# Performance work log

Measured on AMD Instinct MI355X. Metric: run time of the kernel, lower is better.

Reference implementation:

```python
import jax, jax.numpy as jnp
import numpy as np
from jax import lax

EPS = 1e-5

def _ln(x, w, b):
    m = jnp.mean(x, axis=-1, keepdims=True)
    v = jnp.mean((x - m) ** 2, axis=-1, keepdims=True)
    return (x - m) / jnp.sqrt(v + EPS) * w + b

def setup_inputs() -> dict:
    key = jax.random.key(0)
    ks = jax.random.split(key, 16)
    B, H, W, C = 4, 128, 128, 96
    N = H * W
    hidden = 192          # int(2.0 * dim)
    qk = 48               # dim // 2
    x = jax.random.normal(ks[0], (B, N, C), dtype=jnp.float32)
    # LayerNorm params
    norm_w = jnp.ones((C,), jnp.float32); norm_b = jnp.zeros((C,), jnp.float32)
    n1_w = jnp.ones((C,), jnp.float32); n1_b = jnp.zeros((C,), jnp.float32)
    n2_w = jnp.ones((C,), jnp.float32); n2_b = jnp.zeros((C,), jnp.float32)
    # Linear weights stored as [in, out]
    Wh = jax.random.normal(ks[1], (C, hidden), jnp.float32) * 0.02
    bh = jnp.zeros((hidden,), jnp.float32)
    Wqk = jax.random.normal(ks[2], (C, qk), jnp.float32) * 0.02
    bqk = jnp.zeros((qk,), jnp.float32)
    proj_w = jax.random.normal(ks[3], (C, C), jnp.float32) * 0.02
    proj_b = jnp.zeros((C,), jnp.float32)
    # per-branch affine on qk (init: normal std 0.02 / zeros, as in torch code)
    g1 = jax.random.normal(ks[4], (2, qk), jnp.float32) * 0.02
    be1 = jnp.zeros((2, qk), jnp.float32)
    g2 = jax.random.normal(ks[5], (2, qk), jnp.float32) * 0.02
    be2 = jnp.zeros((2, qk), jnp.float32)
    # SR convs (OIHW), kaiming-like init fan_out = k*k*C
    sr1_w = jax.random.normal(ks[6], (C, C, 8, 8), jnp.float32) * np.sqrt(2.0 / (8 * 8 * C))
    sr1_b = jnp.zeros((C,), jnp.float32)
    sr2_w = jax.random.normal(ks[7], (C, C, 4, 4), jnp.float32) * np.sqrt(2.0 / (4 * 4 * C))
    sr2_b = jnp.zeros((C,), jnp.float32)
    return dict(x=x, H=H, W=W, norm_w=norm_w, norm_b=norm_b, Wh=Wh, bh=bh,
                Wqk=Wqk, bqk=bqk, g1=g1, be1=be1, g2=g2, be2=be2,
                sr1_w=sr1_w, sr1_b=sr1_b, sr2_w=sr2_w, sr2_b=sr2_b,
                n1_w=n1_w, n1_b=n1_b, n2_w=n2_w, n2_b=n2_b,
                proj_w=proj_w, proj_b=proj_b)

def _sr_branch(xmap, cw, cb, lw, lb, stride):
    # xmap: [B,C,H,W]; strided conv with kernel==stride, then LN+GELU over tokens
    y = lax.conv_general_dilated(xmap, cw, (stride, stride), 'VALID',
                                 dimension_numbers=('NCHW', 'OIHW', 'NCHW'))
    y = y + cb[:, None, None]
    B, C = y.shape[0], y.shape[1]
    y = y.reshape(B, C, -1).transpose(0, 2, 1)  # [B, N', C]
    return jax.nn.gelu(_ln(y, lw, lb), approximate=False)

def reference(x, H, W, norm_w, norm_b, Wh, bh, Wqk, bqk, g1, be1, g2, be2,
              sr1_w, sr1_b, sr2_w, sr2_b, n1_w, n1_b, n2_w, n2_b, proj_w, proj_b):
    B, N, C = x.shape
    half = C // 2  # C // num_heads with num_heads=2
    nx = _ln(x, norm_w, norm_b)
    h = jax.nn.silu(nx @ Wh + bh)              # [B,N,2C]
    v, gate = h[..., :C], h[..., C:]
    xmap = nx.transpose(0, 2, 1).reshape(B, C, H, W)
    x1 = _sr_branch(xmap, sr1_w, sr1_b, n1_w, n1_b, 8)   # [B, N/64, C]
    x2 = _sr_branch(xmap, sr2_w, sr2_b, n2_w, n2_b, 4)   # [B, N/16, C]
    Z1 = jax.nn.silu(x1 @ Wqk + bqk)           # [B,N1,qk]
    QK1 = Z1[..., None, :] * g1 + be1          # [B,N1,2,qk]
    q1, k1 = QK1[..., 0, :], QK1[..., 1, :]
    Z2 = jax.nn.silu(x2 @ Wqk + bqk)
    QK2 = Z2[..., None, :] * g2 + be2
    q2, k2 = QK2[..., 0, :], QK2[..., 1, :]
    inv_n = 1.0 / N
    a1 = jnp.einsum('bnd,bmd->bnm', v[..., :half], q1) * inv_n
    A1 = jnp.square(jax.nn.relu(a1))
    V1 = jnp.einsum('bnm,bmd->bnd', A1, k1)
    a2 = jnp.einsum('bnd,bmd->bnm', v[..., half:], q2) * inv_n
    A2 = jnp.square(jax.nn.relu(a2))
    V2 = jnp.einsum('bnm,bmd->bnd', A2, k2)
    xc = jnp.concatenate([V1, V2], axis=-1)    # [B,N,C]
    value = xc * gate
    out = value @ proj_w + proj_b
    return out + xc
```

## Files before the change

kernel.cpp:

```cpp
#include <hip/hip_runtime.h>
#include <math.h>

#define NB   4
#define IH   128
#define IW   128
#define NTOK 16384
#define CC   96
#define HID  192
#define QKD  48
#define EPSF 1e-5f
#define INV_N (1.0f/16384.0f)

typedef __attribute__((ext_vector_type(8))) short sh8;
typedef __attribute__((ext_vector_type(4))) short ush4;
typedef __attribute__((ext_vector_type(4))) float f32x4;

__device__ __forceinline__ float wave_sum64(float v){
    #pragma unroll
    for (int off = 32; off > 0; off >>= 1) v += __shfl_xor(v, off, 64);
    return v;
}
__device__ __forceinline__ float siluf(float x){ return x / (1.0f + __expf(-x)); }
__device__ __forceinline__ float geluf(float x){ return 0.5f*x*(1.0f + erff(x*0.7071067811865475f)); }

__device__ __forceinline__ unsigned short f2bf(float f){
    union { float f; unsigned u; } x; x.f = f;
    unsigned u = x.u + 0x7FFFu + ((x.u >> 16) & 1u);
    return (unsigned short)(u >> 16);
}
__device__ __forceinline__ float b2f(unsigned hi16){
    union { unsigned u; float f; } c; c.u = hi16; return c.f;
}
__device__ __forceinline__ unsigned cvtpk(float a, float b){
    unsigned r;
    asm("v_cvt_pk_bf16_f32 %0, %1, %2" : "=v"(r) : "v"(a), "v"(b));
    return r;
}
__device__ __forceinline__ void swap32(unsigned &x, unsigned &y){
    asm volatile("v_permlane32_swap_b32 %0, %1" : "+v"(x), "+v"(y));
}
__device__ __forceinline__ void swap16(unsigned &x, unsigned &y){
    asm volatile("v_permlane16_swap_b32 %0, %1" : "+v"(x), "+v"(y));
}

__global__ __launch_bounds__(256) void k_ln(const float* __restrict__ x,
                                            const float* __restrict__ w,
                                            const float* __restrict__ bb,
                                            unsigned short* __restrict__ nxbf,
                                            unsigned short* __restrict__ nxim,
                                            const float* __restrict__ s1, unsigned short* __restrict__ d1, int n1,
                                            const float* __restrict__ s2, unsigned short* __restrict__ d2, int n2){
    int bid = blockIdx.x;
    if (bid >= 16384){
        int i4 = ((bid - 16384)*256 + threadIdx.x)*4;
        if (i4 < n1){
            float4 v = *(const float4*)(s1 + i4);
            unsigned u0 = cvtpk(v.x, v.y), u1 = cvtpk(v.z, v.w);
            ush4 o = {(short)u0, (short)(u0>>16), (short)u1, (short)(u1>>16)};
            *(ush4*)(d1 + i4) = o;
        } else {
            int j = i4 - n1;
            if (j < n2){
                float4 v = *(const float4*)(s2 + j);
                unsigned u0 = cvtpk(v.x, v.y), u1 = cvtpk(v.z, v.w);
                ush4 o = {(short)u0, (short)(u0>>16), (short)u1, (short)(u1>>16)};
                *(ush4*)(d2 + j) = o;
            }
        }
        return;
    }
    __shared__ unsigned short tile[4][96];
    int r = threadIdx.x >> 6;
    int row = bid*4 + r;
    int l = threadIdx.x & 63;
    const float* xr = x + (size_t)row*CC;
    float a = xr[l];
    float b = (l < 32) ? xr[64+l] : 0.0f;
    float s = wave_sum64(a + b);
    float m = s * (1.0f/96.0f);
    float d1f = a - m;
    float d2f = b - m;
    float sq = d1f*d1f + ((l < 32) ? d2f*d2f : 0.0f);
    float var = wave_sum64(sq) * (1.0f/96.0f);
    float rstd = rsqrtf(var + EPSF);
    unsigned short b1 = f2bf(d1f*rstd*w[l] + bb[l]);
    nxbf[(size_t)row*CC + l] = b1;
    tile[r][l] = b1;
    if (l < 32){
        unsigned short b2 = f2bf(d2f*rstd*w[64+l] + bb[64+l]);
        nxbf[(size_t)row*CC + 64 + l] = b2;
        tile[r][64+l] = b2;
    }
    __syncthreads();
    int t = threadIdx.x;
    if (t < 96){
        int row0 = bid*4;
        int bb2 = row0 >> 14, hw = row0 & 16383;
        ush4 v = {(short)tile[0][t], (short)tile[1][t], (short)tile[2][t], (short)tile[3][t]};
        *(ush4*)(nxim + (((size_t)(bb2*96 + t)) << 14) + hw) = v;
    }
}

__device__ __forceinline__ void conv_body(const unsigned short* __restrict__ nxim,
                                          const unsigned short* __restrict__ wbf,
                                          float* __restrict__ part,
                                          int posLog, int pdimLog, int pszLog,
                                          int kTotal, int rb, int split,
                                          unsigned short* pt, unsigned short* wt){
    const int NCH = 6;
    int tid = threadIdx.x;
    int lane = tid & 63, wid = tid >> 6, lo = lane & 15, g = lane >> 4;
    int psz = 1 << pszLog, pdim = 1 << pdimLog;
    int ksLog = 2*pszLog;
    int kb0 = split * 384;
    int cinc = (64 >> ksLog) << 14;

    int j   = tid & 15;
    int coff = (j*4) >> ksLog;
    int s   = (j*4) & (psz*psz - 1);
    int sy  = s >> pszLog, sx = s & (psz-1);
    int pAddr[4], pOff[4];
    #pragma unroll
    for (int i = 0; i < 4; i++){
        int p = (tid >> 4) + 16*i;
        int R = rb*64 + p;
        int b = R >> posLog, pp = R & ((1 << posLog) - 1);
        int pi = pp >> pdimLog, pj = pp & (pdim-1);
        pAddr[i] = (((b*96 + coff) + (kb0 >> ksLog)) << 14) + (pi*psz + sy)*IW + pj*psz + sx;
        pOff[i]  = p*72 + j*4;
    }
    int jj = tid & 7;
    int wAddr[3], wOff[3];
    #pragma unroll
    for (int i = 0; i < 3; i++){
        int o = (tid >> 3) + 32*i;
        wAddr[i] = o*kTotal + kb0 + jj*8;
        wOff[i]  = o*72 + jj*8;
    }

    f32x4 acc[6];
    #pragma unroll
    for (int ct = 0; ct < 6; ct++) acc[ct] = (f32x4){0.f,0.f,0.f,0.f};

    ush4 pr[4]; sh8 wr[3];
    #pragma unroll
    for (int i = 0; i < 4; i++) pr[i] = *(const ush4*)(nxim + pAddr[i]);
    #pragma unroll
    for (int i = 0; i < 3; i++) wr[i] = *(const sh8*)(wbf + wAddr[i]);

    for (int ch = 0; ch < NCH; ch++){
        __syncthreads();
        #pragma unroll
        for (int i = 0; i < 4; i++) *(ush4*)&pt[pOff[i]] = pr[i];
        #pragma unroll
        for (int i = 0; i < 3; i++) *(sh8*)&wt[wOff[i]] = wr[i];
        if (ch < NCH-1){
            #pragma unroll
            for (int i = 0; i < 4; i++){ pAddr[i] += cinc; pr[i] = *(const ush4*)(nxim + pAddr[i]); }
            #pragma unroll
            for (int i = 0; i < 3; i++){ wAddr[i] += 64;  wr[i] = *(const sh8*)(wbf + wAddr[i]); }
        }
        __syncthreads();

        sh8 a0 = *(const sh8*)&pt[(wid*16 + lo)*72 + g*8];
        sh8 a1 = *(const sh8*)&pt[(wid*16 + lo)*72 + 32 + g*8];
        #pragma unroll
        for (int ct = 0; ct < 6; ct++){
            sh8 b0 = *(const sh8*)&wt[(ct*16 + lo)*72 + g*8];
            sh8 b1 = *(const sh8*)&wt[(ct*16 + lo)*72 + 32 + g*8];
            acc[ct] = __builtin_amdgcn_mfma_f32_16x16x32_bf16(a0, b0, acc[ct], 0, 0, 0);
            acc[ct] = __builtin_amdgcn_mfma_f32_16x16x32_bf16(a1, b1, acc[ct], 0, 0, 0);
        }
    }

    int rowsTotal = NB << posLog;
    #pragma unroll
    for (int ct = 0; ct < 6; ct++){
        int o = ct*16 + lo;
        #pragma unroll
        for (int jx = 0; jx < 4; jx++){
            int R = rb*64 + wid*16 + g*4 + jx;
            part[((size_t)split*rowsTotal + R)*96 + o] = acc[ct][jx];
        }
    }
}

__global__ __launch_bounds__(256) void k_mid(const unsigned short* __restrict__ nxbf,
                                             const unsigned short* __restrict__ nxim,
                                             const float* __restrict__ Wh,
                                             const float* __restrict__ bh,
                                             const unsigned short* __restrict__ w1bf,
                                             const unsigned short* __restrict__ w2bf,
                                             unsigned short* __restrict__ vbuf,
                                             unsigned short* __restrict__ gate,
                                             float* __restrict__ part1,
                                             float* __restrict__ part2){
    __shared__ unsigned short smem[192*100];
    int bid = blockIdx.x;
    if (bid < 512){
        unsigned short* pt = smem;
        unsigned short* wt = smem + 64*72;
        if (bid < 256) conv_body(nxim, w1bf, part1, 8, 4, 3, 6144, bid & 15, bid >> 4, pt, wt);
        else { int b2 = bid - 256; conv_body(nxim, w2bf, part2, 10, 5, 2, 1536, b2 & 63, b2 >> 6, pt, wt); }
        return;
    }
    unsigned short* whbf = smem;
    int tid  = threadIdx.x;
    int lane = tid & 63;
    int wid  = tid >> 6;
    int lo   = lane & 15;
    int g    = lane >> 4;
    int row0 = (bid - 512)*64 + wid*16;

    #pragma unroll
    for (int it = 0; it < 36; it++){
        int pidx = tid + it*256;
        int k = pidx / 96, cp = (pidx - k*96)*2;
        float2 v = *(const float2*)&Wh[k*HID + cp];
        unsigned u = cvtpk(v.x, v.y);
        whbf[cp*100 + k]     = (unsigned short)u;
        whbf[(cp+1)*100 + k] = (unsigned short)(u >> 16);
    }

    sh8 a[3];
    {
        const unsigned short* ar = nxbf + (size_t)(row0 + lo)*CC;
        #pragma unroll
        for (int kc = 0; kc < 3; kc++)
            a[kc] = *(const sh8*)(ar + kc*32 + g*8);
    }
    __syncthreads();

    f32x4 acc[12];
    #pragma unroll
    for (int ct = 0; ct < 12; ct++) acc[ct] = (f32x4){0.f,0.f,0.f,0.f};
    #pragma unroll
    for (int ct = 0; ct < 12; ct++){
        #pragma unroll
        for (int kc = 0; kc < 3; kc++){
            sh8 bw = *(const sh8*)&whbf[(ct*16 + lo)*100 + kc*32 + g*8];
            acc[ct] = __builtin_amdgcn_mfma_f32_16x16x32_bf16(a[kc], bw, acc[ct], 0, 0, 0);
        }
    }

    #pragma unroll
    for (int ct = 0; ct < 12; ct++){
        int col = ct*16 + lo;
        float bcol = bh[col];
        #pragma unroll
        for (int j = 0; j < 4; j++){
            size_t row = row0 + g*4 + j;
            float hv = siluf(acc[ct][j] + bcol);
            unsigned short hb = (unsigned short)cvtpk(hv, hv);
            if (col < 96) vbuf[row*CC + col] = hb;
            else          gate[row*CC + col - 96] = hb;
        }
    }
}

__global__ __launch_bounds__(64) void k_reduce(const float* __restrict__ part1,
                                               const float* __restrict__ part2,
                                               const float* __restrict__ cb1, const float* __restrict__ cb2,
                                               const float* __restrict__ lw1, const float* __restrict__ lw2,
                                               const float* __restrict__ lb1, const float* __restrict__ lb2,
                                               const float* __restrict__ wqk,
                                               const float* __restrict__ bqk,
                                               const float* __restrict__ g1, const float* __restrict__ g2,
                                               const float* __restrict__ be1, const float* __restrict__ be2,
                                               unsigned short* __restrict__ qp1, unsigned short* __restrict__ qp2,
                                               unsigned short* __restrict__ kt1, unsigned short* __restrict__ kt2){
    __shared__ float xsh[96];
    int bid = blockIdx.x;
    bool fst = bid < 1024;
    int row   = fst ? bid : bid - 1024;
    int nsplit= fst ? 16 : 4;
    int rows  = fst ? 1024 : 4096;
    int Mper  = fst ? 256 : 1024;
    const float* part = fst ? part1 : part2;
    const float* cbias= fst ? cb1 : cb2;
    const float* lw   = fst ? lw1 : lw2;
    const float* lb   = fst ? lb1 : lb2;
    const float* g    = fst ? g1 : g2;
    const float* be   = fst ? be1 : be2;
    unsigned short* qp = fst ? qp1 : qp2;
    unsigned short* ktp= fst ? kt1 : kt2;

    int l = threadIdx.x;
    float y1 = 0.0f, y2 = 0.0f;
    for (int s = 0; s < nsplit; s++){
        const float* pr = part + ((size_t)s*rows + row)*96;
        y1 += pr[l];
        if (l < 32) y2 += pr[64+l];
    }
    y1 += cbias[l];
    if (l < 32) y2 += cbias[64+l];
    float s = wave_sum64(y1 + ((l < 32) ? y2 : 0.0f));
    float m = s * (1.0f/96.0f);
    float d1 = y1 - m, d2 = y2 - m;
    float var = wave_sum64(d1*d1 + ((l < 32) ? d2*d2 : 0.0f)) * (1.0f/96.0f);
    float rstd = rsqrtf(var + EPSF);
    xsh[l] = geluf(d1*rstd*lw[l] + lb[l]);
    if (l < 32) xsh[64+l] = geluf(d2*rstd*lw[64+l] + lb[64+l]);
    __syncthreads();
    if (l < 48){
        float z = bqk[l];
        #pragma unroll 4
        for (int c = 0; c < 96; c++) z += xsh[c]*wqk[c*48 + l];
        z = siluf(z);
        float qv = (z*g[l]    + be[l]) * INV_N;
        float kv =  z*g[48+l] + be[48+l];
        int b = row / Mper, p = row - b*Mper;
        qp[(size_t)row*64 + l] = f2bf(qv);
        ktp[((size_t)b*48 + l)*Mper + p] = f2bf(kv);
    } else {
        qp[(size_t)row*64 + l] = 0;
    }
}

__global__ __launch_bounds__(128) void k_attn(const unsigned short* __restrict__ vbuf,
                                              const unsigned short* __restrict__ qp1,
                                              const unsigned short* __restrict__ ktp1,
                                              const unsigned short* __restrict__ qp2,
                                              const unsigned short* __restrict__ ktp2,
                                              unsigned short* __restrict__ V1,
                                              unsigned short* __restrict__ V2){
    __shared__ unsigned short qs[2][32*72];
    __shared__ unsigned short ks[2][48*72];

    int bx   = blockIdx.x;
    int kind = (bx < 512) ? 1 : 0;
    int blk  = (bx < 512) ? bx : bx - 512;
    int tid  = threadIdx.x;
    int wid  = tid >> 6;
    int lane = tid & 63;
    int lo   = lane & 15;
    int g    = lane >> 4;
    int row0 = blk*128 + wid*64;
    int b    = row0 >> 14;

    int   M    = kind ? 1024 : 256;
    const unsigned short* qp = (kind ? qp2 : qp1) + (size_t)b*M*64;
    const unsigned short* kt = (kind ? ktp2 : ktp1) + (size_t)b*48*M;
    int   voff = kind ? 48 : 0;
    unsigned short* vout = kind ? V2 : V1;

    sh8 vb[4][2];
    #pragma unroll
    for (int nt = 0; nt < 4; nt++){
        const unsigned short* vrow = vbuf + (size_t)(row0 + nt*16 + lo)*CC + voff;
        vb[nt][0] = *(const sh8*)(vrow + g*8);
        if (g < 2) vb[nt][1] = *(const sh8*)(vrow + 32 + g*8);
        else { sh8 z = {0,0,0,0,0,0,0,0}; vb[nt][1] = z; }
    }

    int q0r = tid >> 3, q0c = tid & 7;
    int k0d = tid >> 2, k0m = tid & 3;
    bool k2 = tid < 64;

    f32x4 acc[4][3];
    #pragma unroll
    for (int nt = 0; nt < 4; nt++)
        #pragma unroll
        for (int dt = 0; dt < 3; dt++) acc[nt][dt] = (f32x4){0.f,0.f,0.f,0.f};

    int nchunk = M >> 5;
    sh8 qr0 = *(const sh8*)(qp + (size_t)q0r*64 + q0c*8);
    sh8 qr1 = *(const sh8*)(qp + (size_t)(16 + q0r)*64 + q0c*8);
    sh8 kr0 = *(const sh8*)(kt + (size_t)k0d*M + k0m*8);
    sh8 kr1;
    if (k2) kr1 = *(const sh8*)(kt + (size_t)(32 + k0d)*M + k0m*8);

    for (int ch = 0; ch < nchunk; ch++){
        int bs = ch & 1;
        unsigned short* qb = qs[bs];
        unsigned short* kb = ks[bs];
        *(sh8*)&qb[q0r*72 + q0c*8] = qr0;
        *(sh8*)&qb[(16 + q0r)*72 + q0c*8] = qr1;
        *(sh8*)&kb[k0d*72 + k0m*8] = kr0;
        if (k2) *(sh8*)&kb[(32 + k0d)*72 + k0m*8] = kr1;
        __syncthreads();
        if (ch + 1 < nchunk){
            int mb2 = (ch + 1)*32;
            qr0 = *(const sh8*)(qp + (size_t)(mb2 + q0r)*64 + q0c*8);
            qr1 = *(const sh8*)(qp + (size_t)(mb2 + 16 + q0r)*64 + q0c*8);
            kr0 = *(const sh8*)(kt + (size_t)k0d*M + mb2 + k0m*8);
            if (k2) kr1 = *(const sh8*)(kt + (size_t)(32 + k0d)*M + mb2 + k0m*8);
        }

        sh8 aq[2][2];
        #pragma unroll
        for (int mt = 0; mt < 2; mt++)
            #pragma unroll
            for (int kc = 0; kc < 2; kc++)
                aq[mt][kc] = *(const sh8*)&qb[(mt*16 + lo)*72 + kc*32 + g*8];
        f32x4 c[2][4];
        #pragma unroll
        for (int mt = 0; mt < 2; mt++)
            #pragma unroll
            for (int nt = 0; nt < 4; nt++){
                f32x4 cc = (f32x4){0.f,0.f,0.f,0.f};
                cc = __builtin_amdgcn_mfma_f32_16x16x32_bf16(aq[mt][0], vb[nt][0], cc, 0,0,0);
                cc = __builtin_amdgcn_mfma_f32_16x16x32_bf16(aq[mt][1], vb[nt][1], cc, 0,0,0);
                c[mt][nt] = cc;
            }

        sh8 pa[4];
        #pragma unroll
        for (int nt = 0; nt < 4; nt++){
            f32x4 cm0 = c[0][nt];
            f32x4 cm1 = c[1][nt];
            float p00 = fmaxf(cm0[0], 0.f); p00 *= p00;
            float p01 = fmaxf(cm0[1], 0.f); p01 *= p01;
            float p02 = fmaxf(cm0[2], 0.f); p02 *= p02;
            float p03 = fmaxf(cm0[3], 0.f); p03 *= p03;
            float p10 = fmaxf(cm1[0], 0.f); p10 *= p10;
            float p11 = fmaxf(cm1[1], 0.f); p11 *= p11;
            float p12 = fmaxf(cm1[2], 0.f); p12 *= p12;
            float p13 = fmaxf(cm1[3], 0.f); p13 *= p13;
            unsigned a0 = cvtpk(p00, p01);
            unsigned a1 = cvtpk(p02, p03);
            unsigned b0 = cvtpk(p10, p11);
            unsigned b1 = cvtpk(p12, p13);
            swap32(a0, b0); swap16(a0, b0);
            swap32(a1, b1); swap16(a1, b1);
            union { unsigned u[4]; sh8 v; } pk;
            pk.u[0] = a0; pk.u[1] = a1; pk.u[2] = b0; pk.u[3] = b1;
            pa[nt] = pk.v;
        }

        #pragma unroll
        for (int dt = 0; dt < 3; dt++){
            sh8 bk = *(const sh8*)&kb[(dt*16 + lo)*72 + g*8];
            #pragma unroll
            for (int nt = 0; nt < 4; nt++)
                acc[nt][dt] = __builtin_amdgcn_mfma_f32_16x16x32_bf16(pa[nt], bk, acc[nt][dt], 0, 0, 0);
        }
    }

    #pragma unroll
    for (int nt = 0; nt < 4; nt++)
        #pragma unroll
        for (int dt = 0; dt < 3; dt++)
            #pragma unroll
            for (int j = 0; j < 4; j++)
                vout[(size_t)(row0 + nt*16 + g*4 + j)*48 + dt*16 + lo] =
                    (unsigned short)cvtpk(acc[nt][dt][j], acc[nt][dt][j]);
}

__global__ __launch_bounds__(256) void k_final(const unsigned short* __restrict__ V1,
                                               const unsigned short* __restrict__ V2,
                                               const unsigned short* __restrict__ gate,
                                               const float* __restrict__ projw,
                                               const float* __restrict__ projb,
                                               float* __restrict__ out){
    __shared__ unsigned short pjbf[96*100];
    int tid  = threadIdx.x;
    int lane = tid & 63;
    int wid  = tid >> 6;
    int lo   = lane & 15;
    int g    = lane >> 4;
    int row0 = blockIdx.x*64 + wid*16;

    #pragma unroll
    for (int it = 0; it < 18; it++){
        int pidx = tid + it*256;
        int k = pidx / 48, cp = (pidx - k*48)*2;
        float2 v = *(const float2*)&projw[k*CC + cp];
        unsigned u = cvtpk(v.x, v.y);
        pjbf[cp*100 + k]     = (unsigned short)u;
        pjbf[(cp+1)*100 + k] = (unsigned short)(u >> 16);
    }

    sh8 a[3];
    {
        size_t row = row0 + lo;
        const unsigned short* gr = gate + row*CC;
        #pragma unroll
        for (int kc = 0; kc < 3; kc++){
            int d0 = kc*32 + g*8;
            const unsigned short* xsrc = (d0 < 48) ? (V1 + row*48 + d0) : (V2 + row*48 + d0 - 48);
            union { sh8 v; unsigned u[4]; } xu, gu, pk;
            xu.v = *(const sh8*)xsrc;
            gu.v = *(const sh8*)(gr + d0);
            #pragma unroll
            for (int i = 0; i < 4; i++){
                float xl = b2f(xu.u[i] << 16),        xh = b2f(xu.u[i] & 0xffff0000u);
                float gl = b2f(gu.u[i] << 16),        gh = b2f(gu.u[i] & 0xffff0000u);
                pk.u[i] = cvtpk(xl*gl, xh*gh);
            }
            a[kc] = pk.v;
        }
    }
    __syncthreads();

    f32x4 acc[6];
    #pragma unroll
    for (int ct = 0; ct < 6; ct++) acc[ct] = (f32x4){0.f,0.f,0.f,0.f};
    #pragma unroll
    for (int ct = 0; ct < 6; ct++){
        #pragma unroll
        for (int kc = 0; kc < 3; kc++){
            sh8 bw = *(const sh8*)&pjbf[(ct*16 + lo)*100 + kc*32 + g*8];
            acc[ct] = __builtin_amdgcn_mfma_f32_16x16x32_bf16(a[kc], bw, acc[ct], 0, 0, 0);
        }
    }

    #pragma unroll
    for (int ct = 0; ct < 6; ct++){
        int col = ct*16 + lo;
        float bcol = projb[col];
        const unsigned short* xsrc = (ct < 3) ? (V1 + col) : (V2 + col - 48);
        #pragma unroll
        for (int j = 0; j < 4; j++){
            size_t row = row0 + g*4 + j;
            float xc = b2f((unsigned)xsrc[row*48] << 16);
            out[row*CC + col] = acc[ct][j] + bcol + xc;
        }
    }
}

extern "C" void kernel_launch(void* const* d_in, const int* in_sizes, int n_in,
                              void* d_out, int out_size, void* d_ws, size_t ws_size,
                              hipStream_t stream){
    const float* x      = (const float*)d_in[0];
    const float* norm_w = (const float*)d_in[3];
    const float* norm_b = (const float*)d_in[4];
    const float* Wh     = (const float*)d_in[5];
    const float* bh     = (const float*)d_in[6];
    const float* Wqk    = (const float*)d_in[7];
    const float* bqk    = (const float*)d_in[8];
    const float* g1     = (const float*)d_in[9];
    const float* be1    = (const float*)d_in[10];
    const float* g2     = (const float*)d_in[11];
    const float* be2    = (const float*)d_in[12];
    const float* sr1_w  = (const float*)d_in[13];
    const float* sr1_b  = (const float*)d_in[14];
    const float* sr2_w  = (const float*)d_in[15];
    const float* sr2_b  = (const float*)d_in[16];
    const float* n1_w   = (const float*)d_in[17];
    const float* n1_b   = (const float*)d_in[18];
    const float* n2_w   = (const float*)d_in[19];
    const float* n2_b   = (const float*)d_in[20];
    const float* proj_w = (const float*)d_in[21];
    const float* proj_b = (const float*)d_in[22];
    float* out = (float*)d_out;

    float* ws = (float*)d_ws;
    size_t off = 0;
    unsigned short* nxbf = (unsigned short*)(ws + off); off += (size_t)NB*NTOK*CC/2;
    unsigned short* nxim = (unsigned short*)(ws + off); off += (size_t)NB*NTOK*CC/2;
    unsigned short* w1bf = (unsigned short*)(ws + off); off += (size_t)96*6144/2;
    unsigned short* w2bf = (unsigned short*)(ws + off); off += (size_t)96*1536/2;
    unsigned short* vbuf = (unsigned short*)(ws + off); off += (size_t)NB*NTOK*CC/2;
    unsigned short* gate = (unsigned short*)(ws + off); off += (size_t)NB*NTOK*CC/2;
    unsigned short* qp1 = (unsigned short*)(ws + off); off += (size_t)NB*256*64/2;
    unsigned short* kt1 = (unsigned short*)(ws + off); off += (size_t)NB*48*256/2;
    unsigned short* qp2 = (unsigned short*)(ws + off); off += (size_t)NB*1024*64/2;
    unsigned short* kt2 = (unsigned short*)(ws + off); off += (size_t)NB*48*1024/2;
    float* part1= ws + off; off += (size_t)16*NB*256*96;
    float* part2= ws + off; off += (size_t)4*NB*1024*96;
    unsigned short* V1 = (unsigned short*)(ws + off); off += (size_t)NB*NTOK*48/2;
    unsigned short* V2 = (unsigned short*)(ws + off); off += (size_t)NB*NTOK*48/2;
    if (ws_size < off*sizeof(float)) return;

    k_ln   <<<17104, 256, 0, stream>>>(x, norm_w, norm_b, nxbf, nxim,
                                       sr1_w, w1bf, 96*6144, sr2_w, w2bf, 96*1536);
    k_mid  <<<1536, 256, 0, stream>>>(nxbf, nxim, Wh, bh, w1bf, w2bf, vbuf, gate, part1, part2);
    k_reduce<<<5120, 64, 0, stream>>>(part1, part2, sr1_b, sr2_b, n1_w, n2_w, n1_b, n2_b,
                                      Wqk, bqk, g1, g2, be1, be2, qp1, qp2, kt1, kt2);
    k_attn <<<1024, 128, 0, stream>>>(vbuf, qp1, kt1, qp2, kt2, V1, V2);
    k_final<<<1024, 256, 0, stream>>>(V1, V2, gate, proj_w, proj_b, out);
}
```

Before: 134.1 us.

## Retile attention kernel to 4 waves of 32 rows with 64-key chunks

The attention kernel moves from 2 waves of 64 token rows each to 4 waves of 32 rows each per 128-row block. Each iteration now processes 64 keys instead of 32, which halves the number of chunk iterations and barriers. Per-wave register use for the V fragments and accumulators shrinks, which may allow higher occupancy and more parallel waves. In exchange the block uses more shared memory, and each wave reloads the shared Q/K tiles for fewer rows, which lowers per-wave reuse.

Measured after the change: 121.6 us. 1.1x faster.

```diff
diff --git a/kernel.cpp b/kernel.cpp
--- a/kernel.cpp
+++ b/kernel.cpp
@@ -317,14 +317,14 @@
     }
 }
 
-__global__ __launch_bounds__(128) void k_attn(const unsigned short* __restrict__ vbuf,
+__global__ __launch_bounds__(256) void k_attn(const unsigned short* __restrict__ vbuf,
                                               const unsigned short* __restrict__ qp1,
                                               const unsigned short* __restrict__ ktp1,
                                               const unsigned short* __restrict__ qp2,
                                               const unsigned short* __restrict__ ktp2,
                                               unsigned short* __restrict__ V1,
                                               unsigned short* __restrict__ V2){
-    __shared__ unsigned short qs[2][32*72];
+    __shared__ unsigned short qs[2][64*72];
     __shared__ unsigned short ks[2][48*72];
 
     int bx   = blockIdx.x;
@@ -335,7 +335,7 @@
     int lane = tid & 63;
     int lo   = lane & 15;
     int g    = lane >> 4;
-    int row0 = blk*128 + wid*64;
+    int row0 = blk*128 + wid*32;
     int b    = row0 >> 14;
 
     int   M    = kind ? 1024 : 256;
@@ -344,101 +344,104 @@
     int   voff = kind ? 48 : 0;
     unsigned short* vout = kind ? V2 : V1;
 
-    sh8 vb[4][2];
-    #pragma unroll
-    for (int nt = 0; nt < 4; nt++){
+    sh8 vb[2][2];
+    #pragma unroll
+    for (int nt = 0; nt < 2; nt++){
         const unsigned short* vrow = vbuf + (size_t)(row0 + nt*16 + lo)*CC + voff;
         vb[nt][0] = *(const sh8*)(vrow + g*8);
         if (g < 2) vb[nt][1] = *(const sh8*)(vrow + 32 + g*8);
         else { sh8 z = {0,0,0,0,0,0,0,0}; vb[nt][1] = z; }
     }
 
-    int q0r = tid >> 3, q0c = tid & 7;
-    int k0d = tid >> 2, k0m = tid & 3;
-    bool k2 = tid < 64;
-
-    f32x4 acc[4][3];
-    #pragma unroll
-    for (int nt = 0; nt < 4; nt++)
+    int qm_ = tid >> 3, qc_ = tid & 7;
+    int kd_ = tid >> 3, km_ = tid & 7;
+    bool k2 = tid < 128;
+
+    f32x4 acc[2][3];
+    #pragma unroll
+    for (int nt = 0; nt < 2; nt++)
         #pragma unroll
         for (int dt = 0; dt < 3; dt++) acc[nt][dt] = (f32x4){0.f,0.f,0.f,0.f};
 
-    int nchunk = M >> 5;
-    sh8 qr0 = *(const sh8*)(qp + (size_t)q0r*64 + q0c*8);
-    sh8 qr1 = *(const sh8*)(qp + (size_t)(16 + q0r)*64 + q0c*8);
-    sh8 kr0 = *(const sh8*)(kt + (size_t)k0d*M + k0m*8);
+    int nchunk = M >> 6;
+    sh8 qr0 = *(const sh8*)(qp + (size_t)qm_*64 + qc_*8);
+    sh8 qr1 = *(const sh8*)(qp + (size_t)(32 + qm_)*64 + qc_*8);
+    sh8 kr0 = *(const sh8*)(kt + (size_t)kd_*M + km_*8);
     sh8 kr1;
-    if (k2) kr1 = *(const sh8*)(kt + (size_t)(32 + k0d)*M + k0m*8);
+    if (k2) kr1 = *(const sh8*)(kt + (size_t)(32 + kd_)*M + km_*8);
 
     for (int ch = 0; ch < nchunk; ch++){
         int bs = ch & 1;
         unsigned short* qb = qs[bs];
         unsigned short* kb = ks[bs];
-        *(sh8*)&qb[q0r*72 + q0c*8] = qr0;
-        *(sh8*)&qb[(16 + q0r)*72 + q0c*8] = qr1;
-        *(sh8*)&kb[k0d*72 + k0m*8] = kr0;
-        if (k2) *(sh8*)&kb[(32 + k0d)*72 + k0m*8] = kr1;
+        *(sh8*)&qb[qm_*72 + qc_*8] = qr0;
+        *(sh8*)&qb[(32 + qm_)*72 + qc_*8] = qr1;
+        *(sh8*)&kb[kd_*72 + km_*8] = kr0;
+        if (k2) *(sh8*)&kb[(32 + kd_)*72 + km_*8] = kr1;
         __syncthreads();
         if (ch + 1 < nchunk){
-            int mb2 = (ch + 1)*32;
-            qr0 = *(const sh8*)(qp + (size_t)(mb2 + q0r)*64 + q0c*8);
-            qr1 = *(const sh8*)(qp + (size_t)(mb2 + 16 + q0r)*64 + q0c*8);
-            kr0 = *(const sh8*)(kt + (size_t)k0d*M + mb2 + k0m*8);
-            if (k2) kr1 = *(const sh8*)(kt + (size_t)(32 + k0d)*M + mb2 + k0m*8);
-        }
-
-        sh8 aq[2][2];
-        #pragma unroll
-        for (int mt = 0; mt < 2; mt++)
-            #pragma unroll
-            for (int kc = 0; kc < 2; kc++)
-                aq[mt][kc] = *(const sh8*)&qb[(mt*16 + lo)*72 + kc*32 + g*8];
-        f32x4 c[2][4];
-        #pragma unroll
-        for (int mt = 0; mt < 2; mt++)
-            #pragma unroll
-            for (int nt = 0; nt < 4; nt++){
+            int mb2 = (ch + 1)*64;
+            qr0 = *(const sh8*)(qp + (size_t)(mb2 + qm_)*64 + qc_*8);
+            qr1 = *(const sh8*)(qp + (size_t)(mb2 + 32 + qm_)*64 + qc_*8);
+            kr0 = *(const sh8*)(kt + (size_t)kd_*M + mb2 + km_*8);
+            if (k2) kr1 = *(const sh8*)(kt + (size_t)(32 + kd_)*M + mb2 + km_*8);
+        }
+
+        f32x4 c[4][2];
+        #pragma unroll
+        for (int mt = 0; mt < 4; mt++){
+            sh8 aq0 = *(const sh8*)&qb[(mt*16 + lo)*72 + g*8];
+            sh8 aq1 = *(const sh8*)&qb[(mt*16 + lo)*72 + 32 + g*8];
+            #pragma unroll
+            for (int nt = 0; nt < 2; nt++){
                 f32x4 cc = (f32x4){0.f,0.f,0.f,0.f};
-                cc = __builtin_amdgcn_mfma_f32_16x16x32_bf16(aq[mt][0], vb[nt][0], cc, 0,0,0);
-                cc = __builtin_amdgcn_mfma_f32_16x16x32_bf16(aq[mt][1], vb[nt][1], cc, 0,0,0);
+                cc = __builtin_amdgcn_mfma_f32_16x16x32_bf16(aq0, vb[nt][0], cc, 0,0,0);
+                cc = __builtin_amdgcn_mfma_f32_16x16x32_bf16(aq1, vb[nt][1], cc, 0,0,0);
                 c[mt][nt] = cc;
             }
-
-        sh8 pa[4];
-        #pragma unroll
-        for (int nt = 0; nt < 4; nt++){
-            f32x4 cm0 = c[0][nt];
-            f32x4 cm1 = c[1][nt];
-            float p00 = fmaxf(cm0[0], 0.f); p00 *= p00;
-            float p01 = fmaxf(cm0[1], 0.f); p01 *= p01;
-            float p02 = fmaxf(cm0[2], 0.f); p02 *= p02;
-            float p03 = fmaxf(cm0[3], 0.f); p03 *= p03;
-            float p10 = fmaxf(cm1[0], 0.f); p10 *= p10;
-            float p11 = fmaxf(cm1[1], 0.f); p11 *= p11;
-            float p12 = fmaxf(cm1[2], 0.f); p12 *= p12;
-            float p13 = fmaxf(cm1[3], 0.f); p13 *= p13;
-            unsigned a0 = cvtpk(p00, p01);
-            unsigned a1 = cvtpk(p02, p03);
-            unsigned b0 = cvtpk(p10, p11);
-            unsigned b1 = cvtpk(p12, p13);
-            swap32(a0, b0); swap16(a0, b0);
-            swap32(a1, b1); swap16(a1, b1);
-            union { unsigned u[4]; sh8 v; } pk;
-            pk.u[0] = a0; pk.u[1] = a1; pk.u[2] = b0; pk.u[3] = b1;
-            pa[nt] = pk.v;
+        }
+
+        sh8 pa0[2], pa1[2];
+        #pragma unroll
+        for (int nt = 0; nt < 2; nt++){
+            #pragma unroll
+            for (int h = 0; h < 2; h++){
+                f32x4 cm0 = c[h*2][nt];
+                f32x4 cm1 = c[h*2+1][nt];
+                float p00 = fmaxf(cm0[0], 0.f); p00 *= p00;
+                float p01 = fmaxf(cm0[1], 0.f); p01 *= p01;
+                float p02 = fmaxf(cm0[2], 0.f); p02 *= p02;
+                float p03 = fmaxf(cm0[3], 0.f); p03 *= p03;
+                float p10 = fmaxf(cm1[0], 0.f); p10 *= p10;
+                float p11 = fmaxf(cm1[1], 0.f); p11 *= p11;
+                float p12 = fmaxf(cm1[2], 0.f); p12 *= p12;
+                float p13 = fmaxf(cm1[3], 0.f); p13 *= p13;
+                unsigned a0 = cvtpk(p00, p01);
+                unsigned a1 = cvtpk(p02, p03);
+                unsigned b0 = cvtpk(p10, p11);
+                unsigned b1 = cvtpk(p12, p13);
+                swap32(a0, b0); swap16(a0, b0);
+                swap32(a1, b1); swap16(a1, b1);
+                union { unsigned u[4]; sh8 v; } pk;
+                pk.u[0] = a0; pk.u[1] = a1; pk.u[2] = b0; pk.u[3] = b1;
+                if (h == 0) pa0[nt] = pk.v; else pa1[nt] = pk.v;
+            }
         }
 
         #pragma unroll
         for (int dt = 0; dt < 3; dt++){
-            sh8 bk = *(const sh8*)&kb[(dt*16 + lo)*72 + g*8];
-            #pragma unroll
-            for (int nt = 0; nt < 4; nt++)
-                acc[nt][dt] = __builtin_amdgcn_mfma_f32_16x16x32_bf16(pa[nt], bk, acc[nt][dt], 0, 0, 0);
-        }
-    }
-
-    #pragma unroll
-    for (int nt = 0; nt < 4; nt++)
+            sh8 bk0 = *(const sh8*)&kb[(dt*16 + lo)*72 + g*8];
+            sh8 bk1 = *(const sh8*)&kb[(dt*16 + lo)*72 + 32 + g*8];
+            #pragma unroll
+            for (int nt = 0; nt < 2; nt++){
+                acc[nt][dt] = __builtin_amdgcn_mfma_f32_16x16x32_bf16(pa0[nt], bk0, acc[nt][dt], 0, 0, 0);
+                acc[nt][dt] = __builtin_amdgcn_mfma_f32_16x16x32_bf16(pa1[nt], bk1, acc[nt][dt], 0, 0, 0);
+            }
+        }
+    }
+
+    #pragma unroll
+    for (int nt = 0; nt < 2; nt++)
         #pragma unroll
         for (int dt = 0; dt < 3; dt++)
             #pragma unroll
@@ -568,6 +571,6 @@
     k_mid  <<<1536, 256, 0, stream>>>(nxbf, nxim, Wh, bh, w1bf, w2bf, vbuf, gate, part1, part2);
     k_reduce<<<5120, 64, 0, stream>>>(part1, part2, sr1_b, sr2_b, n1_w, n2_w, n1_b, n2_b,
                                       Wqk, bqk, g1, g2, be1, be2, qp1, qp2, kt1, kt2);
-    k_attn <<<1024, 128, 0, stream>>>(vbuf, qp1, kt1, qp2, kt2, V1, V2);
+    k_attn <<<1024, 256, 0, stream>>>(vbuf, qp1, kt1, qp2, kt2, V1, V2);
     k_final<<<1024, 256, 0, stream>>>(V1, V2, gate, proj_w, proj_b, out);
 }
```
